# Kernel optimization log

Measured on AMD Instinct MI355X. Metric: run time of the kernel, lower is better.

Reference implementation:

```python
import jax, jax.numpy as jnp
import numpy as np

N, E, G = 50000, 800000, 64
IN_CH, HID, HEADS, NUM_CLASSES = 128, 64, 4, 10
NEG_SLOPE = 0.2


def _gat_conv(x, src, dst, W, a_src, a_dst, b, concat):
    """PyG-style GATConv with default add_self_loops=True (inference mode)."""
    n = x.shape[0]
    H, C = a_src.shape
    h = (x @ W).reshape(n, H, C)                       # [N,H,C]
    loop = jnp.arange(n, dtype=src.dtype)
    si = jnp.concatenate([src, loop])                  # [E+N]
    di = jnp.concatenate([dst, loop])
    as_n = jnp.sum(h * a_src, axis=-1)                 # [N,H]
    ad_n = jnp.sum(h * a_dst, axis=-1)                 # [N,H]
    e = jax.nn.leaky_relu(as_n[si] + ad_n[di], NEG_SLOPE)   # [E+N,H]
    m = jax.ops.segment_max(e, di, num_segments=n)     # segment softmax (stable)
    ex = jnp.exp(e - m[di])
    denom = jax.ops.segment_sum(ex, di, num_segments=n)
    alpha = ex / (denom[di] + 1e-16)                   # [E+N,H]
    out = jax.ops.segment_sum(alpha[:, :, None] * h[si], di, num_segments=n)  # [N,H,C]
    out = out.reshape(n, H * C) if concat else out.mean(axis=1)
    return out + b


def setup_inputs() -> dict:
    key = jax.random.key(0)
    ks = jax.random.split(key, 20)
    d = {}
    d["x"] = jax.random.normal(ks[0], (N, IN_CH), dtype=jnp.float32)
    d["src"] = jax.random.randint(ks[1], (E,), 0, N, dtype=jnp.int32)
    d["dst"] = jax.random.randint(ks[2], (E,), 0, N, dtype=jnp.int32)
    d["batch"] = jnp.sort(jax.random.randint(ks[3], (N,), 0, G, dtype=jnp.int32))
    s = 0.1
    d["W1"] = jax.random.normal(ks[4], (IN_CH, HEADS * HID), dtype=jnp.float32) * s
    d["as1"] = jax.random.normal(ks[5], (HEADS, HID), dtype=jnp.float32) * s
    d["ad1"] = jax.random.normal(ks[6], (HEADS, HID), dtype=jnp.float32) * s
    d["b1"] = jnp.zeros((HEADS * HID,), jnp.float32)
    d["W2"] = jax.random.normal(ks[7], (HEADS * HID, HEADS * HID), dtype=jnp.float32) * s
    d["as2"] = jax.random.normal(ks[8], (HEADS, HID), dtype=jnp.float32) * s
    d["ad2"] = jax.random.normal(ks[9], (HEADS, HID), dtype=jnp.float32) * s
    d["b2"] = jnp.zeros((HEADS * HID,), jnp.float32)
    # proj: 256 -> 64, heads=1, concat=False
    d["Wp"] = jax.random.normal(ks[10], (HEADS * HID, HID), dtype=jnp.float32) * s
    d["asp"] = jax.random.normal(ks[11], (1, HID), dtype=jnp.float32) * s
    d["adp"] = jax.random.normal(ks[12], (1, HID), dtype=jnp.float32) * s
    d["bp"] = jnp.zeros((HID,), jnp.float32)
    # MLP head
    d["Wh1"] = jax.random.normal(ks[13], (HID, HID), dtype=jnp.float32) * s
    d["bh1"] = jnp.zeros((HID,), jnp.float32)
    d["Wh2"] = jax.random.normal(ks[14], (HID, NUM_CLASSES), dtype=jnp.float32) * s
    d["bh2"] = jnp.zeros((NUM_CLASSES,), jnp.float32)
    return d


def reference(x, src, dst, batch, W1, as1, ad1, b1, W2, as2, ad2, b2,
              Wp, asp, adp, bp, Wh1, bh1, Wh2, bh2):
    h = jax.nn.elu(_gat_conv(x, src, dst, W1, as1, ad1, b1, concat=True))
    h = jax.nn.elu(_gat_conv(h, src, dst, W2, as2, ad2, b2, concat=True))
    h = jax.nn.elu(_gat_conv(h, src, dst, Wp, asp, adp, bp, concat=False))  # [N,HID]
    # global mean pool over graphs
    sums = jax.ops.segment_sum(h, batch, num_segments=G)                    # [G,HID]
    cnt = jax.ops.segment_sum(jnp.ones((h.shape[0],), h.dtype), batch, num_segments=G)
    g = sums / jnp.maximum(cnt, 1.0)[:, None]
    z = jax.nn.relu(g @ Wh1 + bh1)
    return z @ Wh2 + bh2                                                    # [G,NUM_CLASSES]
```

## Files before the change

### kernel.cpp

```cpp
#include <hip/hip_runtime.h>
#include <hip/hip_fp16.h>
#include <cstdint>
#include <cstddef>

#define NNODES 50000
#define NEDGES 800000
#define NGRAPH 64
#define BCAP 128

typedef __attribute__((ext_vector_type(8))) _Float16 half8;
typedef __attribute__((ext_vector_type(4))) float float4v;

__device__ __forceinline__ float lrelu(float x) { return x > 0.f ? x : 0.2f * x; }

__device__ __forceinline__ void wtrans_elem(const float* __restrict__ W,
                                            _Float16* __restrict__ Wt,
                                            int K, int N, int i) {
    int k = i / N, n = i - k * N;
    Wt[(size_t)n * K + k] = (_Float16)W[i];
}

__global__ void prep(const float* __restrict__ W1, const float* __restrict__ W2,
                     const float* __restrict__ Wp, _Float16* __restrict__ w1t,
                     _Float16* __restrict__ w2t, _Float16* __restrict__ wpt,
                     int* __restrict__ cnt) {
    int i = blockIdx.x * blockDim.x + threadIdx.x;
    if (i < 32768) wtrans_elem(W1, w1t, 128, 256, i);
    else if (i < 98304) wtrans_elem(W2, w2t, 256, 256, i - 32768);
    else if (i < 114688) wtrans_elem(Wp, wpt, 256, 64, i - 98304);
    else if (i < 114688 + NNODES) cnt[i - 114688] = 0;
}

__global__ __launch_bounds__(256) void scatter(const int* __restrict__ src,
                                               const int* __restrict__ dst,
                                               int* __restrict__ cnt,
                                               int* __restrict__ bucket) {
    int e = blockIdx.x * 256 + threadIdx.x;
    if (e < NEDGES) {
        int d = dst[e];
        int pos = atomicAdd(&cnt[d], 1);
        if (pos < BCAP) bucket[(size_t)d * BCAP + pos] = src[e];
    }
}

template <int KD, int NFB, int NTOT, int HTOT, bool F32A>
__global__ __launch_bounds__(256) void gemm_lds(const _Float16* __restrict__ A,
                                                const float* __restrict__ A32,
                                                const _Float16* __restrict__ Wt,
                                                const float* __restrict__ a_src,
                                                const float* __restrict__ a_dst,
                                                _Float16* __restrict__ C,
                                                float* __restrict__ as_n,
                                                float* __restrict__ ad_n,
                                                int M) {
    constexpr int NSPLIT = NTOT / (NFB * 16);
    constexpr int HLOC = NFB / 4;
    constexpr int KT = KD / 32;
    constexpr int KC = KD / 8;
    extern __shared__ _Float16 bsm[];

    const int bm = blockIdx.x / NSPLIT;
    const int bn = blockIdx.x % NSPLIT;
    const int tid = threadIdx.x;
    const int w = tid >> 6;
    const int lane = tid & 63;
    const int quad = lane >> 4;
    const int mcol = lane & 15;

    int arow = bm * 64 + w * 16 + mcol;
    if (arow >= M) arow = M - 1;

    half8 areg[KT];
    if constexpr (F32A) {
        const float* ap = A32 + (size_t)arow * KD + quad * 8;
        float4 t[KT * 2];
#pragma unroll
        for (int i = 0; i < KT; ++i) {
            t[2 * i]     = *reinterpret_cast<const float4*>(ap + i * 32);
            t[2 * i + 1] = *reinterpret_cast<const float4*>(ap + i * 32 + 4);
        }
#pragma unroll
        for (int i = 0; i < KT; ++i) {
            areg[i][0] = (_Float16)t[2 * i].x;     areg[i][1] = (_Float16)t[2 * i].y;
            areg[i][2] = (_Float16)t[2 * i].z;     areg[i][3] = (_Float16)t[2 * i].w;
            areg[i][4] = (_Float16)t[2 * i + 1].x; areg[i][5] = (_Float16)t[2 * i + 1].y;
            areg[i][6] = (_Float16)t[2 * i + 1].z; areg[i][7] = (_Float16)t[2 * i + 1].w;
        }
    } else {
        const _Float16* ap = A + (size_t)arow * KD + quad * 8;
#pragma unroll
        for (int i = 0; i < KT; ++i)
            areg[i] = *reinterpret_cast<const half8*>(ap + i * 32);
    }

    constexpr int CHUNKS = NFB * 16 * KC;
    const _Float16* wb = Wt + (size_t)bn * NFB * 16 * KD;
#pragma unroll
    for (int it = 0; it < CHUNKS / 256; ++it) {
        int idx = it * 256 + tid;
        int n = idx / KC, c = idx % KC;
        half8 v = *reinterpret_cast<const half8*>(wb + (size_t)n * KD + c * 8);
        *reinterpret_cast<half8*>(&bsm[n * KD + ((c ^ (n & 7)) * 8)]) = v;
    }
    __syncthreads();

    float4v acc[NFB];
#pragma unroll
    for (int nf = 0; nf < NFB; ++nf) acc[nf] = (float4v)0.f;
#pragma unroll
    for (int i = 0; i < KT; ++i) {
#pragma unroll
        for (int nf = 0; nf < NFB; ++nf) {
            int n = nf * 16 + mcol;
            int ch = (quad + i * 4) ^ (n & 7);
            half8 b = *reinterpret_cast<const half8*>(&bsm[n * KD + ch * 8]);
            acc[nf] = __builtin_amdgcn_mfma_f32_16x16x32_f16(areg[i], b, acc[nf], 0, 0, 0);
        }
    }

    const int orow0 = bm * 64 + w * 16 + quad * 4;
    const int cbase = bn * NFB * 16 + mcol;
#pragma unroll
    for (int r = 0; r < 4; ++r) {
        int orow = orow0 + r;
        if (orow < M) {
            _Float16* crow = C + (size_t)orow * NTOT + cbase;
#pragma unroll
            for (int nf = 0; nf < NFB; ++nf) crow[nf * 16] = (_Float16)acc[nf][r];
        }
    }

    float ps[HLOC][4], pd[HLOC][4];
#pragma unroll
    for (int hd = 0; hd < HLOC; ++hd)
#pragma unroll
        for (int r = 0; r < 4; ++r) { ps[hd][r] = 0.f; pd[hd][r] = 0.f; }
#pragma unroll
    for (int nf = 0; nf < NFB; ++nf) {
        float asv = a_src[bn * NFB * 16 + nf * 16 + mcol];
        float adv = a_dst[bn * NFB * 16 + nf * 16 + mcol];
#pragma unroll
        for (int r = 0; r < 4; ++r) {
            ps[nf >> 2][r] = fmaf(acc[nf][r], asv, ps[nf >> 2][r]);
            pd[nf >> 2][r] = fmaf(acc[nf][r], adv, pd[nf >> 2][r]);
        }
    }
#pragma unroll
    for (int off = 1; off < 16; off <<= 1) {
#pragma unroll
        for (int hd = 0; hd < HLOC; ++hd)
#pragma unroll
            for (int r = 0; r < 4; ++r) {
                ps[hd][r] += __shfl_xor(ps[hd][r], off);
                pd[hd][r] += __shfl_xor(pd[hd][r], off);
            }
    }
    if (mcol == 0) {
#pragma unroll
        for (int r = 0; r < 4; ++r) {
            int orow = orow0 + r;
            if (orow < M) {
#pragma unroll
                for (int hd = 0; hd < HLOC; ++hd) {
                    as_n[orow * HTOT + bn * HLOC + hd] = ps[hd][r];
                    ad_n[orow * HTOT + bn * HLOC + hd] = pd[hd][r];
                }
            }
        }
    }
}

__global__ __launch_bounds__(256) void node_agg2(const int* __restrict__ bucket,
                                                 const int* __restrict__ cnt,
                                                 const __half* __restrict__ h,
                                                 const float* __restrict__ asn,
                                                 const float* __restrict__ adn,
                                                 const float* __restrict__ bias,
                                                 _Float16* __restrict__ outp, int Nn) {
    constexpr int H = 4, HC = 256, EPC = 16;
    const int wid = blockIdx.x * 4 + (threadIdx.x >> 6);
    int n0 = wid * 2;
    if (n0 >= Nn) return;
    int n1 = n0 + 1;
    const bool has1 = (n1 < Nn);
    if (!has1) n1 = n0;
    const int lane = threadIdx.x & 63;
    const int hd = lane >> 4;
    const int ej = lane & 15;
    const int base = lane & 48;
    const int rs0 = n0 * BCAP, rs1 = n1 * BCAP;
    const int re0 = rs0 + min(cnt[n0], BCAP);
    const int re1 = rs1 + min(cnt[n1], BCAP);

    const float ad0 = adn[n0 * H + hd];
    const float ad1 = adn[n1 * H + hd];
    const float es0 = lrelu(asn[n0 * H + hd] + ad0);
    const float es1 = lrelu(asn[n1 * H + hd] + ad1);

    float m0 = es0, m1 = es1;
    float dp0 = (ej == 0) ? 1.f : 0.f;
    float dp1 = dp0;

    float a0, a1, a2, a3, b0, b1, b2, b3;
    {
        uint2 u = *reinterpret_cast<const uint2*>(&h[(size_t)n0 * HC + lane * 4]);
        float2 f0 = __half22float2(*reinterpret_cast<__half2*>(&u.x));
        float2 f1 = __half22float2(*reinterpret_cast<__half2*>(&u.y));
        a0 = f0.x; a1 = f0.y; a2 = f1.x; a3 = f1.y;
    }
    {
        uint2 u = *reinterpret_cast<const uint2*>(&h[(size_t)n1 * HC + lane * 4]);
        float2 f0 = __half22float2(*reinterpret_cast<__half2*>(&u.x));
        float2 f1 = __half22float2(*reinterpret_cast<__half2*>(&u.y));
        b0 = f0.x; b1 = f0.y; b2 = f1.x; b3 = f1.y;
    }

    int c0 = rs0, c1 = rs1;
    while (c0 < re0 || c1 < re1) {
        const int i0 = c0 + ej, i1 = c1 + ej;
        int s0v = 0, s1v = 0;
        float e0 = -1e30f, e1 = -1e30f;
        if (i0 < re0) s0v = bucket[i0];
        if (i1 < re1) s1v = bucket[i1];
        if (i0 < re0) e0 = lrelu(asn[s0v * H + hd] + ad0);
        if (i1 < re1) e1 = lrelu(asn[s1v * H + hd] + ad1);

        float cm0 = e0, cm1 = e1;
#pragma unroll
        for (int off = 1; off < EPC; off <<= 1) {
            cm0 = fmaxf(cm0, __shfl_xor(cm0, off));
            cm1 = fmaxf(cm1, __shfl_xor(cm1, off));
        }
        const float mn0 = fmaxf(m0, cm0);
        const float mn1 = fmaxf(m1, cm1);
        const float sc0 = __expf(m0 - mn0);
        const float sc1 = __expf(m1 - mn1);
        m0 = mn0; m1 = mn1;
        dp0 *= sc0; dp1 *= sc1;
        a0 *= sc0; a1 *= sc0; a2 *= sc0; a3 *= sc0;
        b0 *= sc1; b1 *= sc1; b2 *= sc1; b3 *= sc1;
        const float x0 = __expf(e0 - m0);
        const float x1 = __expf(e1 - m1);
        dp0 += x0; dp1 += x1;

        auto bodyA = [&](int j) {
            float ex = __shfl(x0, base + j);
            int sj = __shfl(s0v, base + j);
            uint2 u = *reinterpret_cast<const uint2*>(&h[(size_t)sj * HC + lane * 4]);
            float2 f0 = __half22float2(*reinterpret_cast<__half2*>(&u.x));
            float2 f1 = __half22float2(*reinterpret_cast<__half2*>(&u.y));
            a0 = fmaf(ex, f0.x, a0);
            a1 = fmaf(ex, f0.y, a1);
            a2 = fmaf(ex, f1.x, a2);
            a3 = fmaf(ex, f1.y, a3);
        };
        auto bodyB = [&](int j) {
            float ex = __shfl(x1, base + j);
            int sj = __shfl(s1v, base + j);
            uint2 u = *reinterpret_cast<const uint2*>(&h[(size_t)sj * HC + lane * 4]);
            float2 f0 = __half22float2(*reinterpret_cast<__half2*>(&u.x));
            float2 f1 = __half22float2(*reinterpret_cast<__half2*>(&u.y));
            b0 = fmaf(ex, f0.x, b0);
            b1 = fmaf(ex, f0.y, b1);
            b2 = fmaf(ex, f1.x, b2);
            b3 = fmaf(ex, f1.y, b3);
        };

        const int nA = min(EPC, re0 - c0);
        const int nB = min(EPC, re1 - c1);
        const int nmax = max(nA, nB);
        if (nmax == EPC) {
#pragma unroll
            for (int j = 0; j < EPC; ++j) { bodyA(j); bodyB(j); }
        } else {
#pragma unroll 4
            for (int j = 0; j < nmax; ++j) { bodyA(j); bodyB(j); }
        }
        c0 += EPC; c1 += EPC;
    }

#pragma unroll
    for (int off = 1; off < EPC; off <<= 1) {
        dp0 += __shfl_xor(dp0, off);
        dp1 += __shfl_xor(dp1, off);
    }
    const float inv0 = 1.f / (dp0 + 1e-16f);
    const float inv1 = 1.f / (dp1 + 1e-16f);

    {
        float v0 = a0 * inv0 + bias[lane * 4 + 0];
        float v1 = a1 * inv0 + bias[lane * 4 + 1];
        float v2 = a2 * inv0 + bias[lane * 4 + 2];
        float v3 = a3 * inv0 + bias[lane * 4 + 3];
        v0 = v0 > 0.f ? v0 : expm1f(v0);
        v1 = v1 > 0.f ? v1 : expm1f(v1);
        v2 = v2 > 0.f ? v2 : expm1f(v2);
        v3 = v3 > 0.f ? v3 : expm1f(v3);
        union { _Float16 h4[4]; uint2 u; } r;
        r.h4[0] = (_Float16)v0; r.h4[1] = (_Float16)v1;
        r.h4[2] = (_Float16)v2; r.h4[3] = (_Float16)v3;
        reinterpret_cast<uint2*>(outp + (size_t)n0 * HC)[lane] = r.u;
    }
    if (has1) {
        float v0 = b0 * inv1 + bias[lane * 4 + 0];
        float v1 = b1 * inv1 + bias[lane * 4 + 1];
        float v2 = b2 * inv1 + bias[lane * 4 + 2];
        float v3 = b3 * inv1 + bias[lane * 4 + 3];
        v0 = v0 > 0.f ? v0 : expm1f(v0);
        v1 = v1 > 0.f ? v1 : expm1f(v1);
        v2 = v2 > 0.f ? v2 : expm1f(v2);
        v3 = v3 > 0.f ? v3 : expm1f(v3);
        union { _Float16 h4[4]; uint2 u; } r;
        r.h4[0] = (_Float16)v0; r.h4[1] = (_Float16)v1;
        r.h4[2] = (_Float16)v2; r.h4[3] = (_Float16)v3;
        reinterpret_cast<uint2*>(outp + (size_t)n1 * HC)[lane] = r.u;
    }
}

__global__ __launch_bounds__(256) void node_aggP(const int* __restrict__ bucket,
                                                 const int* __restrict__ cnt,
                                                 const __half* __restrict__ h,
                                                 const float* __restrict__ asn,
                                                 const float* __restrict__ adn,
                                                 const float* __restrict__ bias,
                                                 _Float16* __restrict__ outp, int Nn) {
    constexpr int HC = 64, EPC = 16;
    const int wv = threadIdx.x >> 6;
    const int lane = threadIdx.x & 63;
    const int li = lane & 15;
    const int gb = lane & 48;
    const int n = blockIdx.x * 16 + wv * 4 + (lane >> 4);
    if (n >= Nn) return;

    const int rs = n * BCAP;
    const int re = rs + min(cnt[n], BCAP);
    const float ad = adn[n];
    float m = lrelu(asn[n] + ad);
    float dp = (li == 0) ? 1.f : 0.f;

    float a0, a1, a2, a3;
    {
        uint2 u = *reinterpret_cast<const uint2*>(&h[(size_t)n * HC + li * 4]);
        float2 f0 = __half22float2(*reinterpret_cast<__half2*>(&u.x));
        float2 f1 = __half22float2(*reinterpret_cast<__half2*>(&u.y));
        a0 = f0.x; a1 = f0.y; a2 = f1.x; a3 = f1.y;
    }

    auto body = [&](int j, float x, int sv) {
        float ex = __shfl(x, gb + j);
        int sj = __shfl(sv, gb + j);
        uint2 u = *reinterpret_cast<const uint2*>(&h[(size_t)sj * HC + li * 4]);
        float2 f0 = __half22float2(*reinterpret_cast<__half2*>(&u.x));
        float2 f1 = __half22float2(*reinterpret_cast<__half2*>(&u.y));
        a0 = fmaf(ex, f0.x, a0);
        a1 = fmaf(ex, f0.y, a1);
        a2 = fmaf(ex, f1.x, a2);
        a3 = fmaf(ex, f1.y, a3);
    };

    for (int c = rs; c < re; c += EPC) {
        int i = c + li;
        int sv = 0;
        float e = -1e30f;
        if (i < re) {
            sv = bucket[i];
            e = lrelu(asn[sv] + ad);
        }
        float cm = e;
#pragma unroll
        for (int off = 1; off < EPC; off <<= 1) cm = fmaxf(cm, __shfl_xor(cm, off));
        float mn = fmaxf(m, cm);
        float sc = __expf(m - mn);
        m = mn;
        dp *= sc;
        a0 *= sc; a1 *= sc; a2 *= sc; a3 *= sc;
        float x = __expf(e - m);
        dp += x;
        const int nb2 = min(EPC, re - c);
        if (nb2 == EPC) {
#pragma unroll
            for (int j = 0; j < EPC; ++j) body(j, x, sv);
        } else {
#pragma unroll 4
            for (int j = 0; j < nb2; ++j) body(j, x, sv);
        }
    }
#pragma unroll
    for (int off = 1; off < EPC; off <<= 1) dp += __shfl_xor(dp, off);
    const float inv = 1.f / (dp + 1e-16f);
    float v0 = a0 * inv + bias[li * 4 + 0];
    float v1 = a1 * inv + bias[li * 4 + 1];
    float v2 = a2 * inv + bias[li * 4 + 2];
    float v3 = a3 * inv + bias[li * 4 + 3];
    v0 = v0 > 0.f ? v0 : expm1f(v0);
    v1 = v1 > 0.f ? v1 : expm1f(v1);
    v2 = v2 > 0.f ? v2 : expm1f(v2);
    v3 = v3 > 0.f ? v3 : expm1f(v3);
    union { _Float16 h4[4]; uint2 u; } r;
    r.h4[0] = (_Float16)v0; r.h4[1] = (_Float16)v1;
    r.h4[2] = (_Float16)v2; r.h4[3] = (_Float16)v3;
    *reinterpret_cast<uint2*>(&outp[(size_t)n * HC + li * 4]) = r.u;
}

__global__ __launch_bounds__(256) void pool_mlp(const __half* __restrict__ feat,
                                                const int* __restrict__ batch,
                                                const float* __restrict__ Wh1,
                                                const float* __restrict__ bh1,
                                                const float* __restrict__ Wh2,
                                                const float* __restrict__ bh2,
                                                float* __restrict__ out, int Nn) {
    __shared__ float swsum[4][64];
    __shared__ float smean[64];
    __shared__ float shid[64];
    const int g = blockIdx.x;
    const int tid = threadIdx.x;
    const int lane = tid & 63;
    const int w = tid >> 6;
    int lo = 0, hi = Nn;
    while (lo < hi) { int mid = (lo + hi) >> 1; if (batch[mid] < g) lo = mid + 1; else hi = mid; }
    const int start = lo;
    hi = Nn;
    while (lo < hi) { int mid = (lo + hi) >> 1; if (batch[mid] < g + 1) lo = mid + 1; else hi = mid; }
    const int end = lo;
    float acc = 0.f;
    for (int n = start + w; n < end; n += 4) acc += __half2float(feat[(size_t)n * 64 + lane]);
    swsum[w][lane] = acc;
    __syncthreads();
    if (w == 0) {
        float s = swsum[0][lane] + swsum[1][lane] + swsum[2][lane] + swsum[3][lane];
        float c = (float)(end - start);
        c = c > 1.f ? c : 1.f;
        smean[lane] = s / c;
    }
    __syncthreads();
    if (tid < 64) {
        float a = bh1[tid];
        for (int k = 0; k < 64; ++k) a = fmaf(smean[k], Wh1[k * 64 + tid], a);
        shid[tid] = a > 0.f ? a : 0.f;
    }
    __syncthreads();
    if (tid < 10) {
        float a = bh2[tid];
        for (int k = 0; k < 64; ++k) a = fmaf(shid[k], Wh2[k * 10 + tid], a);
        out[g * 10 + tid] = a;
    }
}

extern "C" void kernel_launch(void* const* d_in, const int* in_sizes, int n_in,
                              void* d_out, int out_size, void* d_ws, size_t ws_size,
                              hipStream_t stream) {
    const float* x   = (const float*)d_in[0];
    const int* src   = (const int*)d_in[1];
    const int* dst   = (const int*)d_in[2];
    const int* batch = (const int*)d_in[3];
    const float* W1  = (const float*)d_in[4];
    const float* as1 = (const float*)d_in[5];
    const float* ad1 = (const float*)d_in[6];
    const float* b1  = (const float*)d_in[7];
    const float* W2  = (const float*)d_in[8];
    const float* as2 = (const float*)d_in[9];
    const float* ad2 = (const float*)d_in[10];
    const float* b2  = (const float*)d_in[11];
    const float* Wp  = (const float*)d_in[12];
    const float* asp = (const float*)d_in[13];
    const float* adp = (const float*)d_in[14];
    const float* bp  = (const float*)d_in[15];
    const float* Wh1 = (const float*)d_in[16];
    const float* bh1 = (const float*)d_in[17];
    const float* Wh2 = (const float*)d_in[18];
    const float* bh2 = (const float*)d_in[19];
    float* out = (float*)d_out;

    _Float16* hbase = (_Float16*)d_ws;
    const size_t NHC = (size_t)NNODES * 256;
    _Float16* ha16  = hbase;
    _Float16* hb16  = ha16 + NHC;
    _Float16* projh = hb16 + NHC;
    _Float16* w1t   = projh + (size_t)NNODES * 64;
    _Float16* w2t   = w1t + 256 * 128;
    _Float16* wpt   = w2t + 256 * 256;
    float* asn = (float*)(wpt + 64 * 256);
    float* adn = asn + (size_t)NNODES * 4;
    int* cnt    = (int*)(adn + (size_t)NNODES * 4);
    int* bucket = cnt + NNODES;

    const int gemmGrid = (NNODES + 63) / 64;
    const int scatGrid = (NEDGES + 255) / 256;
    const int agg2Grid = ((NNODES + 1) / 2 + 3) / 4;
    const int aggPGrid = (NNODES + 15) / 16;

    prep<<<(114688 + NNODES + 255) / 256, 256, 0, stream>>>(W1, W2, Wp, w1t, w2t, wpt, cnt);
    scatter<<<scatGrid, 256, 0, stream>>>(src, dst, cnt, bucket);
    gemm_lds<128, 8, 256, 4, true><<<gemmGrid * 2, 256, 32768, stream>>>(
        nullptr, x, w1t, as1, ad1, ha16, asn, adn, NNODES);
    node_agg2<<<agg2Grid, 256, 0, stream>>>(bucket, cnt,
        (const __half*)ha16, asn, adn, b1, hb16, NNODES);
    gemm_lds<256, 8, 256, 4, false><<<gemmGrid * 2, 256, 65536, stream>>>(
        hb16, nullptr, w2t, as2, ad2, ha16, asn, adn, NNODES);
    node_agg2<<<agg2Grid, 256, 0, stream>>>(bucket, cnt,
        (const __half*)ha16, asn, adn, b2, hb16, NNODES);
    gemm_lds<256, 4, 64, 1, false><<<gemmGrid, 256, 32768, stream>>>(
        hb16, nullptr, wpt, asp, adp, ha16, asn, adn, NNODES);
    node_aggP<<<aggPGrid, 256, 0, stream>>>(bucket, cnt,
        (const __half*)ha16, asn, adn, bp, projh, NNODES);
    pool_mlp<<<NGRAPH, 256, 0, stream>>>((const __half*)projh, batch, Wh1, bh1, Wh2, bh2, out, NNODES);
}
```

Measured before the change: 457.4 us.

## Use two-pass softmax in node_agg2 and shrink GEMM tile width

Replaces the online-softmax loop in node_agg2 with a two-pass scheme. All bucketed neighbor indices and scores, up to BCAP, are first loaded into registers, then the global max and normalized weights are computed, and the feature gather accumulates with pre-normalized weights. This drops the per-chunk rescaling of the accumulators and the serial max/exp dependency between chunks, at the cost of more registers for the per-node arrays. The first two GEMM launches also switch to a narrower column tile with twice as many blocks and half the LDS.

```diff
diff --git a/kernel.cpp b/kernel.cpp
--- a/kernel.cpp
+++ b/kernel.cpp
@@ -177,7 +177,7 @@
                                                  const float* __restrict__ adn,
                                                  const float* __restrict__ bias,
                                                  _Float16* __restrict__ outp, int Nn) {
-    constexpr int H = 4, HC = 256, EPC = 16;
+    constexpr int H = 4, HC = 256, EPC = 16, NB = BCAP / EPC;
     const int wid = blockIdx.x * 4 + (threadIdx.x >> 6);
     int n0 = wid * 2;
     if (n0 >= Nn) return;
@@ -197,55 +197,75 @@
     const float es0 = lrelu(asn[n0 * H + hd] + ad0);
     const float es1 = lrelu(asn[n1 * H + hd] + ad1);
 
+    int sv0[NB], sv1[NB];
+    float e0[NB], e1[NB];
     float m0 = es0, m1 = es1;
-    float dp0 = (ej == 0) ? 1.f : 0.f;
-    float dp1 = dp0;
-
+#pragma unroll
+    for (int b = 0; b < NB; ++b) {
+        const int i0 = rs0 + b * EPC + ej;
+        const int i1 = rs1 + b * EPC + ej;
+        sv0[b] = 0; sv1[b] = 0;
+        e0[b] = -1e30f; e1[b] = -1e30f;
+        if (i0 < re0) sv0[b] = bucket[i0];
+        if (i1 < re1) sv1[b] = bucket[i1];
+        if (i0 < re0) e0[b] = lrelu(asn[sv0[b] * H + hd] + ad0);
+        if (i1 < re1) e1[b] = lrelu(asn[sv1[b] * H + hd] + ad1);
+        m0 = fmaxf(m0, e0[b]);
+        m1 = fmaxf(m1, e1[b]);
+    }
+#pragma unroll
+    for (int off = 1; off < EPC; off <<= 1) {
+        m0 = fmaxf(m0, __shfl_xor(m0, off));
+        m1 = fmaxf(m1, __shfl_xor(m1, off));
+    }
+
+    float dl0 = (ej == 0) ? __expf(es0 - m0) : 0.f;
+    float dl1 = (ej == 0) ? __expf(es1 - m1) : 0.f;
+#pragma unroll
+    for (int b = 0; b < NB; ++b) {
+        const float x0 = __expf(e0[b] - m0);
+        const float x1 = __expf(e1[b] - m1);
+        e0[b] = x0; e1[b] = x1;
+        dl0 += x0; dl1 += x1;
+    }
+#pragma unroll
+    for (int off = 1; off < EPC; off <<= 1) {
+        dl0 += __shfl_xor(dl0, off);
+        dl1 += __shfl_xor(dl1, off);
+    }
+    const float inv0 = 1.f / (dl0 + 1e-16f);
+    const float inv1 = 1.f / (dl1 + 1e-16f);
+#pragma unroll
+    for (int b = 0; b < NB; ++b) { e0[b] *= inv0; e1[b] *= inv1; }
+
+    const float ws0 = __expf(es0 - m0) * inv0;
+    const float ws1 = __expf(es1 - m1) * inv1;
     float a0, a1, a2, a3, b0, b1, b2, b3;
     {
         uint2 u = *reinterpret_cast<const uint2*>(&h[(size_t)n0 * HC + lane * 4]);
         float2 f0 = __half22float2(*reinterpret_cast<__half2*>(&u.x));
         float2 f1 = __half22float2(*reinterpret_cast<__half2*>(&u.y));
-        a0 = f0.x; a1 = f0.y; a2 = f1.x; a3 = f1.y;
+        a0 = ws0 * f0.x; a1 = ws0 * f0.y; a2 = ws0 * f1.x; a3 = ws0 * f1.y;
     }
     {
         uint2 u = *reinterpret_cast<const uint2*>(&h[(size_t)n1 * HC + lane * 4]);
         float2 f0 = __half22float2(*reinterpret_cast<__half2*>(&u.x));
         float2 f1 = __half22float2(*reinterpret_cast<__half2*>(&u.y));
-        b0 = f0.x; b1 = f0.y; b2 = f1.x; b3 = f1.y;
-    }
-
-    int c0 = rs0, c1 = rs1;
-    while (c0 < re0 || c1 < re1) {
-        const int i0 = c0 + ej, i1 = c1 + ej;
-        int s0v = 0, s1v = 0;
-        float e0 = -1e30f, e1 = -1e30f;
-        if (i0 < re0) s0v = bucket[i0];
-        if (i1 < re1) s1v = bucket[i1];
-        if (i0 < re0) e0 = lrelu(asn[s0v * H + hd] + ad0);
-        if (i1 < re1) e1 = lrelu(asn[s1v * H + hd] + ad1);
-
-        float cm0 = e0, cm1 = e1;
-#pragma unroll
-        for (int off = 1; off < EPC; off <<= 1) {
-            cm0 = fmaxf(cm0, __shfl_xor(cm0, off));
-            cm1 = fmaxf(cm1, __shfl_xor(cm1, off));
-        }
-        const float mn0 = fmaxf(m0, cm0);
-        const float mn1 = fmaxf(m1, cm1);
-        const float sc0 = __expf(m0 - mn0);
-        const float sc1 = __expf(m1 - mn1);
-        m0 = mn0; m1 = mn1;
-        dp0 *= sc0; dp1 *= sc1;
-        a0 *= sc0; a1 *= sc0; a2 *= sc0; a3 *= sc0;
-        b0 *= sc1; b1 *= sc1; b2 *= sc1; b3 *= sc1;
-        const float x0 = __expf(e0 - m0);
-        const float x1 = __expf(e1 - m1);
-        dp0 += x0; dp1 += x1;
+        b0 = ws1 * f0.x; b1 = ws1 * f0.y; b2 = ws1 * f1.x; b3 = ws1 * f1.y;
+    }
+
+#pragma unroll
+    for (int b = 0; b < NB; ++b) {
+        const int c0 = rs0 + b * EPC;
+        const int c1 = rs1 + b * EPC;
+        const int nA = (c0 < re0) ? min(EPC, re0 - c0) : 0;
+        const int nB2 = (c1 < re1) ? min(EPC, re1 - c1) : 0;
+        const int nmax = max(nA, nB2);
+        if (nmax == 0) continue;
 
         auto bodyA = [&](int j) {
-            float ex = __shfl(x0, base + j);
-            int sj = __shfl(s0v, base + j);
+            float ex = __shfl(e0[b], base + j);
+            int sj = __shfl(sv0[b], base + j);
             uint2 u = *reinterpret_cast<const uint2*>(&h[(size_t)sj * HC + lane * 4]);
             float2 f0 = __half22float2(*reinterpret_cast<__half2*>(&u.x));
             float2 f1 = __half22float2(*reinterpret_cast<__half2*>(&u.y));
@@ -255,8 +275,8 @@
             a3 = fmaf(ex, f1.y, a3);
         };
         auto bodyB = [&](int j) {
-            float ex = __shfl(x1, base + j);
-            int sj = __shfl(s1v, base + j);
+            float ex = __shfl(e1[b], base + j);
+            int sj = __shfl(sv1[b], base + j);
             uint2 u = *reinterpret_cast<const uint2*>(&h[(size_t)sj * HC + lane * 4]);
             float2 f0 = __half22float2(*reinterpret_cast<__half2*>(&u.x));
             float2 f1 = __half22float2(*reinterpret_cast<__half2*>(&u.y));
@@ -266,9 +286,6 @@
             b3 = fmaf(ex, f1.y, b3);
         };
 
-        const int nA = min(EPC, re0 - c0);
-        const int nB = min(EPC, re1 - c1);
-        const int nmax = max(nA, nB);
         if (nmax == EPC) {
 #pragma unroll
             for (int j = 0; j < EPC; ++j) { bodyA(j); bodyB(j); }
@@ -276,22 +293,13 @@
 #pragma unroll 4
             for (int j = 0; j < nmax; ++j) { bodyA(j); bodyB(j); }
         }
-        c0 += EPC; c1 += EPC;
-    }
-
-#pragma unroll
-    for (int off = 1; off < EPC; off <<= 1) {
-        dp0 += __shfl_xor(dp0, off);
-        dp1 += __shfl_xor(dp1, off);
-    }
-    const float inv0 = 1.f / (dp0 + 1e-16f);
-    const float inv1 = 1.f / (dp1 + 1e-16f);
+    }
 
     {
-        float v0 = a0 * inv0 + bias[lane * 4 + 0];
-        float v1 = a1 * inv0 + bias[lane * 4 + 1];
-        float v2 = a2 * inv0 + bias[lane * 4 + 2];
-        float v3 = a3 * inv0 + bias[lane * 4 + 3];
+        float v0 = a0 + bias[lane * 4 + 0];
+        float v1 = a1 + bias[lane * 4 + 1];
+        float v2 = a2 + bias[lane * 4 + 2];
+        float v3 = a3 + bias[lane * 4 + 3];
         v0 = v0 > 0.f ? v0 : expm1f(v0);
         v1 = v1 > 0.f ? v1 : expm1f(v1);
         v2 = v2 > 0.f ? v2 : expm1f(v2);
@@ -302,10 +310,10 @@
         reinterpret_cast<uint2*>(outp + (size_t)n0 * HC)[lane] = r.u;
     }
     if (has1) {
-        float v0 = b0 * inv1 + bias[lane * 4 + 0];
-        float v1 = b1 * inv1 + bias[lane * 4 + 1];
-        float v2 = b2 * inv1 + bias[lane * 4 + 2];
-        float v3 = b3 * inv1 + bias[lane * 4 + 3];
+        float v0 = b0 + bias[lane * 4 + 0];
+        float v1 = b1 + bias[lane * 4 + 1];
+        float v2 = b2 + bias[lane * 4 + 2];
+        float v3 = b3 + bias[lane * 4 + 3];
         v0 = v0 > 0.f ? v0 : expm1f(v0);
         v1 = v1 > 0.f ? v1 : expm1f(v1);
         v2 = v2 > 0.f ? v2 : expm1f(v2);
@@ -491,11 +499,11 @@
 
     prep<<<(114688 + NNODES + 255) / 256, 256, 0, stream>>>(W1, W2, Wp, w1t, w2t, wpt, cnt);
     scatter<<<scatGrid, 256, 0, stream>>>(src, dst, cnt, bucket);
-    gemm_lds<128, 8, 256, 4, true><<<gemmGrid * 2, 256, 32768, stream>>>(
+    gemm_lds<128, 4, 256, 4, true><<<gemmGrid * 4, 256, 16384, stream>>>(
         nullptr, x, w1t, as1, ad1, ha16, asn, adn, NNODES);
     node_agg2<<<agg2Grid, 256, 0, stream>>>(bucket, cnt,
         (const __half*)ha16, asn, adn, b1, hb16, NNODES);
-    gemm_lds<256, 8, 256, 4, false><<<gemmGrid * 2, 256, 65536, stream>>>(
+    gemm_lds<256, 4, 256, 4, false><<<gemmGrid * 4, 256, 32768, stream>>>(
         hb16, nullptr, w2t, as2, ad2, ha16, asn, adn, NNODES);
     node_agg2<<<agg2Grid, 256, 0, stream>>>(bucket, cnt,
         (const __half*)ha16, asn, adn, b2, hb16, NNODES);
```

After: 501.1 us. 1.1x slower.

## Fuse edge scatter into first GEMM launch, pre-convert x to fp16, narrow GEMM N tiles

Applied to the files above, without the earlier changes.

The edge bucketing scatter now runs inside the same launch as the first-layer GEMM, with block index deciding the role, so the atomic scatter can overlap with the GEMM. The fp32→fp16 conversion of x moves into the prep kernel, which writes it into the hb16 buffer so the GEMM reads fp16 directly. The layer-1 and layer-2 GEMMs switch from 8 to 4 N-fragments per block with four N-splits, halving LDS per block to raise occupancy. The cost is an extra full write and read of x in fp16, and more blocks that each reload the A rows.

```diff
diff --git a/kernel.cpp b/kernel.cpp
--- a/kernel.cpp
+++ b/kernel.cpp
@@ -21,31 +21,134 @@
 }
 
 __global__ void prep(const float* __restrict__ W1, const float* __restrict__ W2,
-                     const float* __restrict__ Wp, _Float16* __restrict__ w1t,
-                     _Float16* __restrict__ w2t, _Float16* __restrict__ wpt,
+                     const float* __restrict__ Wp, const float* __restrict__ x,
+                     _Float16* __restrict__ w1t, _Float16* __restrict__ w2t,
+                     _Float16* __restrict__ wpt, _Float16* __restrict__ xh,
                      int* __restrict__ cnt) {
     int i = blockIdx.x * blockDim.x + threadIdx.x;
     if (i < 32768) wtrans_elem(W1, w1t, 128, 256, i);
     else if (i < 98304) wtrans_elem(W2, w2t, 256, 256, i - 32768);
     else if (i < 114688) wtrans_elem(Wp, wpt, 256, 64, i - 98304);
-    else if (i < 114688 + NNODES) cnt[i - 114688] = 0;
-}
-
-__global__ __launch_bounds__(256) void scatter(const int* __restrict__ src,
-                                               const int* __restrict__ dst,
-                                               int* __restrict__ cnt,
-                                               int* __restrict__ bucket) {
-    int e = blockIdx.x * 256 + threadIdx.x;
-    if (e < NEDGES) {
-        int d = dst[e];
-        int pos = atomicAdd(&cnt[d], 1);
-        if (pos < BCAP) bucket[(size_t)d * BCAP + pos] = src[e];
-    }
-}
-
-template <int KD, int NFB, int NTOT, int HTOT, bool F32A>
+    else if (i < 164688) cnt[i - 114688] = 0;
+    else {
+        int j = i - 164688;
+        if (j < NNODES * 128) xh[j] = (_Float16)x[j];
+    }
+}
+
+template <int KD, int NFB, int NTOT, int HTOT>
+__device__ __forceinline__ void gemm_lds_body(const _Float16* __restrict__ A,
+                                              const _Float16* __restrict__ Wt,
+                                              const float* __restrict__ a_src,
+                                              const float* __restrict__ a_dst,
+                                              _Float16* __restrict__ C,
+                                              float* __restrict__ as_n,
+                                              float* __restrict__ ad_n,
+                                              int M, int blk) {
+    constexpr int NSPLIT = NTOT / (NFB * 16);
+    constexpr int HLOC = NFB / 4;
+    constexpr int KT = KD / 32;
+    constexpr int KC = KD / 8;
+    extern __shared__ _Float16 bsm[];
+
+    const int bm = blk / NSPLIT;
+    const int bn = blk % NSPLIT;
+    const int tid = threadIdx.x;
+    const int w = tid >> 6;
+    const int lane = tid & 63;
+    const int quad = lane >> 4;
+    const int mcol = lane & 15;
+
+    int arow = bm * 64 + w * 16 + mcol;
+    if (arow >= M) arow = M - 1;
+
+    half8 areg[KT];
+    {
+        const _Float16* ap = A + (size_t)arow * KD + quad * 8;
+#pragma unroll
+        for (int i = 0; i < KT; ++i)
+            areg[i] = *reinterpret_cast<const half8*>(ap + i * 32);
+    }
+
+    constexpr int CHUNKS = NFB * 16 * KC;
+    const _Float16* wb = Wt + (size_t)bn * NFB * 16 * KD;
+#pragma unroll
+    for (int it = 0; it < CHUNKS / 256; ++it) {
+        int idx = it * 256 + tid;
+        int n = idx / KC, c = idx % KC;
+        half8 v = *reinterpret_cast<const half8*>(wb + (size_t)n * KD + c * 8);
+        *reinterpret_cast<half8*>(&bsm[n * KD + ((c ^ (n & 7)) * 8)]) = v;
+    }
+    __syncthreads();
+
+    float4v acc[NFB];
+#pragma unroll
+    for (int nf = 0; nf < NFB; ++nf) acc[nf] = (float4v)0.f;
+#pragma unroll
+    for (int i = 0; i < KT; ++i) {
+#pragma unroll
+        for (int nf = 0; nf < NFB; ++nf) {
+            int n = nf * 16 + mcol;
+            int ch = (quad + i * 4) ^ (n & 7);
+            half8 b = *reinterpret_cast<const half8*>(&bsm[n * KD + ch * 8]);
+            acc[nf] = __builtin_amdgcn_mfma_f32_16x16x32_f16(areg[i], b, acc[nf], 0, 0, 0);
+        }
+    }
+
+    const int orow0 = bm * 64 + w * 16 + quad * 4;
+    const int cbase = bn * NFB * 16 + mcol;
+#pragma unroll
+    for (int r = 0; r < 4; ++r) {
+        int orow = orow0 + r;
+        if (orow < M) {
+            _Float16* crow = C + (size_t)orow * NTOT + cbase;
+#pragma unroll
+            for (int nf = 0; nf < NFB; ++nf) crow[nf * 16] = (_Float16)acc[nf][r];
+        }
+    }
+
+    float ps[HLOC][4], pd[HLOC][4];
+#pragma unroll
+    for (int hd = 0; hd < HLOC; ++hd)
+#pragma unroll
+        for (int r = 0; r < 4; ++r) { ps[hd][r] = 0.f; pd[hd][r] = 0.f; }
+#pragma unroll
+    for (int nf = 0; nf < NFB; ++nf) {
+        float asv = a_src[bn * NFB * 16 + nf * 16 + mcol];
+        float adv = a_dst[bn * NFB * 16 + nf * 16 + mcol];
+#pragma unroll
+        for (int r = 0; r < 4; ++r) {
+            ps[nf >> 2][r] = fmaf(acc[nf][r], asv, ps[nf >> 2][r]);
+            pd[nf >> 2][r] = fmaf(acc[nf][r], adv, pd[nf >> 2][r]);
+        }
+    }
+#pragma unroll
+    for (int off = 1; off < 16; off <<= 1) {
+#pragma unroll
+        for (int hd = 0; hd < HLOC; ++hd)
+#pragma unroll
+            for (int r = 0; r < 4; ++r) {
+                ps[hd][r] += __shfl_xor(ps[hd][r], off);
+                pd[hd][r] += __shfl_xor(pd[hd][r], off);
+            }
+    }
+    if (mcol == 0) {
+#pragma unroll
+        for (int r = 0; r < 4; ++r) {
+            int orow = orow0 + r;
+            if (orow < M) {
+#pragma unroll
+                for (int hd = 0; hd < HLOC; ++hd) {
+                    as_n[orow * HTOT + bn * HLOC + hd] = ps[hd][r];
+                    ad_n[orow * HTOT + bn * HLOC + hd] = pd[hd][r];
+                }
+            }
+        }
+    }
+}
+
+template <int KD, int NFB, int NTOT, int HTOT>
 __global__ __launch_bounds__(256) void gemm_lds(const _Float16* __restrict__ A,
-                                                const float* __restrict__ A32,
                                                 const _Float16* __restrict__ Wt,
                                                 const float* __restrict__ a_src,
                                                 const float* __restrict__ a_dst,
@@ -53,119 +156,30 @@
                                                 float* __restrict__ as_n,
                                                 float* __restrict__ ad_n,
                                                 int M) {
-    constexpr int NSPLIT = NTOT / (NFB * 16);
-    constexpr int HLOC = NFB / 4;
-    constexpr int KT = KD / 32;
-    constexpr int KC = KD / 8;
-    extern __shared__ _Float16 bsm[];
-
-    const int bm = blockIdx.x / NSPLIT;
-    const int bn = blockIdx.x % NSPLIT;
-    const int tid = threadIdx.x;
-    const int w = tid >> 6;
-    const int lane = tid & 63;
-    const int quad = lane >> 4;
-    const int mcol = lane & 15;
-
-    int arow = bm * 64 + w * 16 + mcol;
-    if (arow >= M) arow = M - 1;
-
-    half8 areg[KT];
-    if constexpr (F32A) {
-        const float* ap = A32 + (size_t)arow * KD + quad * 8;
-        float4 t[KT * 2];
-#pragma unroll
-        for (int i = 0; i < KT; ++i) {
-            t[2 * i]     = *reinterpret_cast<const float4*>(ap + i * 32);
-            t[2 * i + 1] = *reinterpret_cast<const float4*>(ap + i * 32 + 4);
-        }
-#pragma unroll
-        for (int i = 0; i < KT; ++i) {
-            areg[i][0] = (_Float16)t[2 * i].x;     areg[i][1] = (_Float16)t[2 * i].y;
-            areg[i][2] = (_Float16)t[2 * i].z;     areg[i][3] = (_Float16)t[2 * i].w;
-            areg[i][4] = (_Float16)t[2 * i + 1].x; areg[i][5] = (_Float16)t[2 * i + 1].y;
-            areg[i][6] = (_Float16)t[2 * i + 1].z; areg[i][7] = (_Float16)t[2 * i + 1].w;
-        }
+    gemm_lds_body<KD, NFB, NTOT, HTOT>(A, Wt, a_src, a_dst, C, as_n, ad_n, M, blockIdx.x);
+}
+
+__global__ __launch_bounds__(256) void gemm1_scatter(const _Float16* __restrict__ xh,
+                                                     const _Float16* __restrict__ w1t,
+                                                     const float* __restrict__ a_src,
+                                                     const float* __restrict__ a_dst,
+                                                     _Float16* __restrict__ C,
+                                                     float* __restrict__ as_n,
+                                                     float* __restrict__ ad_n,
+                                                     const int* __restrict__ src,
+                                                     const int* __restrict__ dst,
+                                                     int* __restrict__ cnt,
+                                                     int* __restrict__ bucket,
+                                                     int gemmBlocks) {
+    if ((int)blockIdx.x < gemmBlocks) {
+        gemm_lds_body<128, 4, 256, 4>(xh, w1t, a_src, a_dst, C, as_n, ad_n,
+                                      NNODES, blockIdx.x);
     } else {
-        const _Float16* ap = A + (size_t)arow * KD + quad * 8;
-#pragma unroll
-        for (int i = 0; i < KT; ++i)
-            areg[i] = *reinterpret_cast<const half8*>(ap + i * 32);
-    }
-
-    constexpr int CHUNKS = NFB * 16 * KC;
-    const _Float16* wb = Wt + (size_t)bn * NFB * 16 * KD;
-#pragma unroll
-    for (int it = 0; it < CHUNKS / 256; ++it) {
-        int idx = it * 256 + tid;
-        int n = idx / KC, c = idx % KC;
-        half8 v = *reinterpret_cast<const half8*>(wb + (size_t)n * KD + c * 8);
-        *reinterpret_cast<half8*>(&bsm[n * KD + ((c ^ (n & 7)) * 8)]) = v;
-    }
-    __syncthreads();
-
-    float4v acc[NFB];
-#pragma unroll
-    for (int nf = 0; nf < NFB; ++nf) acc[nf] = (float4v)0.f;
-#pragma unroll
-    for (int i = 0; i < KT; ++i) {
-#pragma unroll
-        for (int nf = 0; nf < NFB; ++nf) {
-            int n = nf * 16 + mcol;
-            int ch = (quad + i * 4) ^ (n & 7);
-            half8 b = *reinterpret_cast<const half8*>(&bsm[n * KD + ch * 8]);
-            acc[nf] = __builtin_amdgcn_mfma_f32_16x16x32_f16(areg[i], b, acc[nf], 0, 0, 0);
-        }
-    }
-
-    const int orow0 = bm * 64 + w * 16 + quad * 4;
-    const int cbase = bn * NFB * 16 + mcol;
-#pragma unroll
-    for (int r = 0; r < 4; ++r) {
-        int orow = orow0 + r;
-        if (orow < M) {
-            _Float16* crow = C + (size_t)orow * NTOT + cbase;
-#pragma unroll
-            for (int nf = 0; nf < NFB; ++nf) crow[nf * 16] = (_Float16)acc[nf][r];
-        }
-    }
-
-    float ps[HLOC][4], pd[HLOC][4];
-#pragma unroll
-    for (int hd = 0; hd < HLOC; ++hd)
-#pragma unroll
-        for (int r = 0; r < 4; ++r) { ps[hd][r] = 0.f; pd[hd][r] = 0.f; }
-#pragma unroll
-    for (int nf = 0; nf < NFB; ++nf) {
-        float asv = a_src[bn * NFB * 16 + nf * 16 + mcol];
-        float adv = a_dst[bn * NFB * 16 + nf * 16 + mcol];
-#pragma unroll
-        for (int r = 0; r < 4; ++r) {
-            ps[nf >> 2][r] = fmaf(acc[nf][r], asv, ps[nf >> 2][r]);
-            pd[nf >> 2][r] = fmaf(acc[nf][r], adv, pd[nf >> 2][r]);
-        }
-    }
-#pragma unroll
-    for (int off = 1; off < 16; off <<= 1) {
-#pragma unroll
-        for (int hd = 0; hd < HLOC; ++hd)
-#pragma unroll
-            for (int r = 0; r < 4; ++r) {
-                ps[hd][r] += __shfl_xor(ps[hd][r], off);
-                pd[hd][r] += __shfl_xor(pd[hd][r], off);
-            }
-    }
-    if (mcol == 0) {
-#pragma unroll
-        for (int r = 0; r < 4; ++r) {
-            int orow = orow0 + r;
-            if (orow < M) {
-#pragma unroll
-                for (int hd = 0; hd < HLOC; ++hd) {
-                    as_n[orow * HTOT + bn * HLOC + hd] = ps[hd][r];
-                    ad_n[orow * HTOT + bn * HLOC + hd] = pd[hd][r];
-                }
-            }
+        int e = (blockIdx.x - gemmBlocks) * 256 + threadIdx.x;
+        if (e < NEDGES) {
+            int d = dst[e];
+            int pos = atomicAdd(&cnt[d], 1);
+            if (pos < BCAP) bucket[(size_t)d * BCAP + pos] = src[e];
         }
     }
 }
@@ -483,24 +497,25 @@
     float* adn = asn + (size_t)NNODES * 4;
     int* cnt    = (int*)(adn + (size_t)NNODES * 4);
     int* bucket = cnt + NNODES;
+    _Float16* xh = hb16;
 
     const int gemmGrid = (NNODES + 63) / 64;
     const int scatGrid = (NEDGES + 255) / 256;
     const int agg2Grid = ((NNODES + 1) / 2 + 3) / 4;
     const int aggPGrid = (NNODES + 15) / 16;
 
-    prep<<<(114688 + NNODES + 255) / 256, 256, 0, stream>>>(W1, W2, Wp, w1t, w2t, wpt, cnt);
-    scatter<<<scatGrid, 256, 0, stream>>>(src, dst, cnt, bucket);
-    gemm_lds<128, 8, 256, 4, true><<<gemmGrid * 2, 256, 32768, stream>>>(
-        nullptr, x, w1t, as1, ad1, ha16, asn, adn, NNODES);
+    prep<<<(164688 + NNODES * 128 + 255) / 256, 256, 0, stream>>>(
+        W1, W2, Wp, x, w1t, w2t, wpt, xh, cnt);
+    gemm1_scatter<<<gemmGrid * 4 + scatGrid, 256, 16384, stream>>>(
+        xh, w1t, as1, ad1, ha16, asn, adn, src, dst, cnt, bucket, gemmGrid * 4);
     node_agg2<<<agg2Grid, 256, 0, stream>>>(bucket, cnt,
         (const __half*)ha16, asn, adn, b1, hb16, NNODES);
-    gemm_lds<256, 8, 256, 4, false><<<gemmGrid * 2, 256, 65536, stream>>>(
-        hb16, nullptr, w2t, as2, ad2, ha16, asn, adn, NNODES);
+    gemm_lds<256, 4, 256, 4><<<gemmGrid * 4, 256, 32768, stream>>>(
+        hb16, w2t, as2, ad2, ha16, asn, adn, NNODES);
     node_agg2<<<agg2Grid, 256, 0, stream>>>(bucket, cnt,
         (const __half*)ha16, asn, adn, b2, hb16, NNODES);
-    gemm_lds<256, 4, 64, 1, false><<<gemmGrid, 256, 32768, stream>>>(
-        hb16, nullptr, wpt, asp, adp, ha16, asn, adn, NNODES);
+    gemm_lds<256, 4, 64, 1><<<gemmGrid, 256, 32768, stream>>>(
+        hb16, wpt, asp, adp, ha16, asn, adn, NNODES);
     node_aggP<<<aggPGrid, 256, 0, stream>>>(bucket, cnt,
         (const __half*)ha16, asn, adn, bp, projh, NNODES);
     pool_mlp<<<NGRAPH, 256, 0, stream>>>((const __half*)projh, batch, Wh1, bh1, Wh2, bh2, out, NNODES);
```

Result: slower. 472.5 us (+3.3%).
